# Kernel optimization log

Hardware: AMD Instinct MI355X
Metric: run time of the kernel (lower is better)

The kernel has to match this reference:

```python
import jax, jax.numpy as jnp
import numpy as np

H = 1024
NUM_HEADS = 16
HEAD_DIM = H // NUM_HEADS
EPS = 1e-6
GEN_E, GEN_IE = 8, 4096 // 8     # general experts, per-expert intermediate
MOD_E, MOD_IE = 4, 4096 // 4     # per-modality experts, per-expert intermediate


def layernorm(x, g, b):
    m = jnp.mean(x, axis=-1, keepdims=True)
    v = jnp.mean((x - m) ** 2, axis=-1, keepdims=True)
    return (x - m) * jax.lax.rsqrt(v + EPS) * g + b


def attention(x, qkv_w, qkv_b, proj_w, proj_b):
    B, N, _ = x.shape
    qkv = (x @ qkv_w + qkv_b).reshape(B, N, 3, NUM_HEADS, HEAD_DIM)
    qkv = jnp.transpose(qkv, (2, 0, 3, 1, 4))  # [3,B,h,N,d]
    q, k, v = qkv[0], qkv[1], qkv[2]
    scale = HEAD_DIM ** -0.5
    attn = jax.nn.softmax(jnp.einsum('bhnd,bhmd->bhnm', q, k) * scale, axis=-1)
    out = jnp.einsum('bhnm,bhmd->bhnd', attn, v)
    out = jnp.transpose(out, (0, 2, 1, 3)).reshape(B, N, H)
    return out @ proj_w + proj_b


def routed_mlp(x, position_ids, gate_up, down, ie):
    # expert_id = position % num_experts; compute all experts then select per token
    # (avoids materializing per-token [T,H,2I] gathered weights).
    E = gate_up.shape[0]
    eids = position_ids % E  # [B,N]
    gu = jnp.einsum('bnh,ehi->bnei', x, gate_up)              # [B,N,E,2*ie]
    gu = jnp.take_along_axis(gu, eids[..., None, None], axis=2)[:, :, 0]
    gate, up = gu[..., :ie], gu[..., ie:]
    inter = jax.nn.silu(gate) * up                             # [B,N,ie]
    dn = jnp.einsum('bni,eih->bneh', inter, down)              # [B,N,E,H]
    return jnp.take_along_axis(dn, eids[..., None, None], axis=2)[:, :, 0]


def setup_inputs() -> dict:
    key = jax.random.key(0)
    ks = jax.random.split(key, 16)
    B, N = 2, 2048
    inp = {
        'x': jax.random.normal(ks[0], (B, N, H), jnp.float32),
        'qkv_w': jax.random.normal(ks[1], (H, 3 * H), jnp.float32) * 0.02,
        'qkv_b': jnp.zeros((3 * H,), jnp.float32),
        'proj_w': jax.random.normal(ks[2], (H, H), jnp.float32) * 0.02,
        'proj_b': jnp.zeros((H,), jnp.float32),
        'ln1_g': jnp.ones((H,), jnp.float32), 'ln1_b': jnp.zeros((H,), jnp.float32),
        'ln2_g': jnp.ones((H,), jnp.float32), 'ln2_b': jnp.zeros((H,), jnp.float32),
        'ln3_g': jnp.ones((H,), jnp.float32), 'ln3_b': jnp.zeros((H,), jnp.float32),
        'gen_gu': jax.random.normal(ks[3], (GEN_E, H, 2 * GEN_IE), jnp.float32) * 0.02,
        'gen_dn': jax.random.normal(ks[4], (GEN_E, GEN_IE, H), jnp.float32) * 0.02,
        'text_gu': jax.random.normal(ks[5], (MOD_E, H, 2 * MOD_IE), jnp.float32) * 0.02,
        'text_dn': jax.random.normal(ks[6], (MOD_E, MOD_IE, H), jnp.float32) * 0.02,
        'img_gu': jax.random.normal(ks[7], (MOD_E, H, 2 * MOD_IE), jnp.float32) * 0.02,
        'img_dn': jax.random.normal(ks[8], (MOD_E, MOD_IE, H), jnp.float32) * 0.02,
        'aud_gu': jax.random.normal(ks[9], (MOD_E, H, 2 * MOD_IE), jnp.float32) * 0.02,
        'aud_dn': jax.random.normal(ks[10], (MOD_E, MOD_IE, H), jnp.float32) * 0.02,
        'vid_gu': jax.random.normal(ks[11], (MOD_E, H, 2 * MOD_IE), jnp.float32) * 0.02,
        'vid_dn': jax.random.normal(ks[12], (MOD_E, MOD_IE, H), jnp.float32) * 0.02,
        'modality_ids': jax.random.randint(ks[13], (B, N), 0, 4, jnp.int32),
        'position_ids': jnp.arange(B * N, dtype=jnp.int32).reshape(B, N),
    }
    return inp


def reference(x, qkv_w, qkv_b, proj_w, proj_b,
              ln1_g, ln1_b, ln2_g, ln2_b, ln3_g, ln3_b,
              gen_gu, gen_dn, text_gu, text_dn, img_gu, img_dn,
              aud_gu, aud_dn, vid_gu, vid_dn,
              modality_ids, position_ids):
    x = x + attention(layernorm(x, ln1_g, ln1_b), qkv_w, qkv_b, proj_w, proj_b)
    x = x + routed_mlp(layernorm(x, ln2_g, ln2_b), position_ids, gen_gu, gen_dn, GEN_IE)
    normed = layernorm(x, ln3_g, ln3_b)
    tm = (modality_ids == 0)[..., None].astype(x.dtype)
    im = (modality_ids == 1)[..., None].astype(x.dtype)
    am = (modality_ids == 2)[..., None].astype(x.dtype)
    vm = (modality_ids == 3)[..., None].astype(x.dtype)
    x = x + (routed_mlp(normed, position_ids, text_gu, text_dn, MOD_IE) * tm
             + routed_mlp(normed, position_ids, img_gu, img_dn, MOD_IE) * im
             + routed_mlp(normed, position_ids, aud_gu, aud_dn, MOD_IE) * am
             + routed_mlp(normed, position_ids, vid_gu, vid_dn, MOD_IE) * vm)
    return x
```

## Files before the change

### kernel.cpp

```cpp
#include <hip/hip_runtime.h>

#define T_TOKENS 4096
#define HDIM 1024

typedef __attribute__((ext_vector_type(8))) short bf16x8;
typedef __attribute__((ext_vector_type(4))) float f32x4;

#define EXP2F(x) __builtin_amdgcn_exp2f(x)

static __device__ inline unsigned short f2bf(float f) {
  unsigned u = __float_as_uint(f);
  unsigned r = (u + 0x7FFFu + ((u >> 16) & 1u)) >> 16;
  return (unsigned short)r;
}
static __device__ __forceinline__ unsigned cvtpk(float lo, float hi) {
  unsigned r;
  asm("v_cvt_pk_bf16_f32 %0, %1, %2" : "=v"(r) : "v"(lo), "v"(hi));
  return r;
}
static __device__ __forceinline__ void gl16(const void* g, void* l) {
  __builtin_amdgcn_global_load_lds((const __attribute__((address_space(1))) void*)g,
                                   (__attribute__((address_space(3))) void*)l, 16, 0, 0);
}

__launch_bounds__(256)
__global__ void ln_kernel(const float* __restrict__ in, const float* __restrict__ g,
                          const float* __restrict__ b, unsigned short* __restrict__ out) {
  const int row = blockIdx.x;
  const int tid = threadIdx.x;
  const long base = (long)row * HDIM;
  float4 v = *(const float4*)(in + base + tid * 4);
  __shared__ float red[256];
  red[tid] = v.x + v.y + v.z + v.w;
  __syncthreads();
  for (int st = 128; st > 0; st >>= 1) {
    if (tid < st) red[tid] += red[tid + st];
    __syncthreads();
  }
  const float mean = red[0] * (1.f / HDIM);
  __syncthreads();
  const float dx = v.x - mean, dy = v.y - mean, dz = v.z - mean, dw = v.w - mean;
  red[tid] = dx * dx + dy * dy + dz * dz + dw * dw;
  __syncthreads();
  for (int st = 128; st > 0; st >>= 1) {
    if (tid < st) red[tid] += red[tid + st];
    __syncthreads();
  }
  const float rstd = rsqrtf(red[0] * (1.f / HDIM) + 1e-6f);
  const int c = tid * 4;
  const float4 g4 = *(const float4*)(g + c);
  const float4 b4 = *(const float4*)(b + c);
  uint2 o;
  o.x = cvtpk(dx * rstd * g4.x + b4.x, dy * rstd * g4.y + b4.y);
  o.y = cvtpk(dz * rstd * g4.z + b4.z, dw * rstd * g4.w + b4.w);
  *(uint2*)(out + base + c) = o;
}

__launch_bounds__(256)
__global__ void build_groups(const int* __restrict__ pids, const int* __restrict__ mids,
                             int* __restrict__ gen_cnt, int* __restrict__ gen_list,
                             int* __restrict__ mod_cnt, int* __restrict__ mod_list) {
  const int t = blockIdx.x * 256 + threadIdx.x;
  if (t >= T_TOKENS) return;
  const int p = pids[t];
  const int ge = p & 7;
  int s = atomicAdd(&gen_cnt[ge], 1);
  if (s < 512) gen_list[ge * 512 + s] = t;
  const int g = mids[t] * 4 + (p & 3);
  s = atomicAdd(&mod_cnt[g], 1);
  if (s < 1024) mod_list[g * 1024 + s] = t;
}

__launch_bounds__(256)
__global__ void convert_w(const float* __restrict__ W, unsigned short* __restrict__ Wt,
                          int K, int N) {
  const long zo = (long)blockIdx.z * K * N;
  const float* Wp = W + zo;
  unsigned short* Wo = Wt + zo;
  const int n0 = blockIdx.x * 64, k0 = blockIdx.y * 64;
  __shared__ float T[64][65];
  const int tid = threadIdx.x;
#pragma unroll
  for (int i = 0; i < 4; ++i) {
    const int item = tid + i * 256;
    const int kk = item >> 4, c4 = (item & 15) * 4;
    const float4 v = *(const float4*)(Wp + (long)(k0 + kk) * N + n0 + c4);
    T[c4 + 0][kk] = v.x; T[c4 + 1][kk] = v.y; T[c4 + 2][kk] = v.z; T[c4 + 3][kk] = v.w;
  }
  __syncthreads();
#pragma unroll
  for (int i = 0; i < 4; ++i) {
    const int item = tid + i * 256;
    const int nn = item >> 4, k4 = (item & 15) * 4;
    uint2 p;
    p.x = cvtpk(T[nn][k4 + 0], T[nn][k4 + 1]);
    p.y = cvtpk(T[nn][k4 + 2], T[nn][k4 + 3]);
    *(uint2*)(Wo + (long)(n0 + nn) * K + k0 + k4) = p;
  }
}

enum { MODE_DENSE = 0, MODE_GEN = 1, MODE_MOD = 2 };
enum { OM_F32R = 0, OM_BF16 = 1, OM_QKV = 2 };

template <int MODE, int OMODE, bool WBF16, bool BIAS>
__launch_bounds__(256)
__global__ void mgemm(const unsigned short* __restrict__ A,
                      const void* __restrict__ w0, const float* __restrict__ w1,
                      const float* __restrict__ w2, const float* __restrict__ w3,
                      long wstep, const float* __restrict__ bias,
                      const float* __restrict__ resid, void* __restrict__ Cout,
                      unsigned short* __restrict__ qb, unsigned short* __restrict__ kb,
                      unsigned short* __restrict__ vtb,
                      int K, int N,
                      const int* __restrict__ cnts, const int* __restrict__ rowlist,
                      int cap) {
  const int z = blockIdx.z;
  const int n0 = blockIdx.x * 128;
  const int m0 = blockIdx.y * 128;

  int Meff = 1 << 30;
  const int* list = nullptr;
  if constexpr (MODE != MODE_DENSE) {
    Meff = cnts[z];
    if (m0 >= Meff) return;
    list = rowlist + z * cap;
  }

  __shared__ char As[128 * 64 * 2];
  __shared__ char Bs[128 * 64 * 2];

  const int tid = threadIdx.x;
  const int w = tid >> 6;
  const int lane = tid & 63;
  const int wm = w >> 1, wn = w & 1;
  const int srow = lane >> 3, sc = lane & 7;

  const unsigned short* asrc[4];
  char* aldsb = As + w * 4096;
#pragma unroll
  for (int i = 0; i < 4; ++i) {
    const int r = w * 32 + i * 8 + srow;
    long tok;
    if constexpr (MODE == MODE_DENSE) {
      tok = m0 + r;
    } else {
      int gm = m0 + r;
      if (gm >= Meff) gm = Meff - 1;
      tok = (long)list[gm];
    }
    asrc[i] = A + tok * (long)K + (sc ^ (r & 7)) * 8;
  }

  const unsigned short* bsrc[4];
  char* bldsb = Bs + w * 4096;
  const float* bptr[4];
  int boff[4];
  if constexpr (WBF16) {
    const unsigned short* W = (const unsigned short*)w0;
    if constexpr (MODE != MODE_DENSE) W += (long)z * wstep;
#pragma unroll
    for (int i = 0; i < 4; ++i) {
      const int r = w * 32 + i * 8 + srow;
      bsrc[i] = W + (long)(n0 + r) * K + (sc ^ (r & 7)) * 8;
    }
  } else {
    const float* W;
    if constexpr (MODE == MODE_MOD) {
      const int mm = z >> 2;
      const float* basep = (mm == 0) ? (const float*)w0 : (mm == 1) ? w1 : (mm == 2) ? w2 : w3;
      W = basep + (long)(z & 3) * wstep;
    } else {
      W = (const float*)w0 + (MODE != MODE_DENSE ? (long)z * wstep : 0);
    }
#pragma unroll
    for (int j = 0; j < 4; ++j) {
      const int item = tid + j * 256;
      const int kc = item >> 7;
      const int nl = item & 127;
      bptr[j] = W + (long)(kc * 8) * N + n0 + nl;
      boff[j] = (nl * 128 + kc * 16) ^ ((nl & 7) << 4);
    }
  }

  f32x4 acc[4][4] = {};

  for (int kt = 0; kt < K; kt += 64) {
    __syncthreads();
#pragma unroll
    for (int i = 0; i < 4; ++i) gl16(asrc[i] + kt, aldsb + i * 1024);
    if constexpr (WBF16) {
#pragma unroll
      for (int i = 0; i < 4; ++i) gl16(bsrc[i] + kt, bldsb + i * 1024);
    } else {
#pragma unroll
      for (int j = 0; j < 4; ++j) {
        const float* bp = bptr[j] + (long)kt * N;
        float kv[8];
#pragma unroll
        for (int u = 0; u < 8; ++u) kv[u] = bp[(long)u * N];
        uint4 p;
        p.x = cvtpk(kv[0], kv[1]);
        p.y = cvtpk(kv[2], kv[3]);
        p.z = cvtpk(kv[4], kv[5]);
        p.w = cvtpk(kv[6], kv[7]);
        *(uint4*)(Bs + boff[j]) = p;
      }
    }
    __syncthreads();

#pragma unroll
    for (int kk = 0; kk < 2; ++kk) {
      const int kb2 = kk * 64 + (lane >> 4) * 16;
      bf16x8 af[4], bfr[4];
#pragma unroll
      for (int f = 0; f < 4; ++f) {
        const int ar = wm * 64 + f * 16 + (lane & 15);
        af[f] = *(bf16x8*)(As + ((ar * 128 + kb2) ^ ((ar & 7) << 4)));
        const int br = wn * 64 + f * 16 + (lane & 15);
        bfr[f] = *(bf16x8*)(Bs + ((br * 128 + kb2) ^ ((br & 7) << 4)));
      }
#pragma unroll
      for (int mf = 0; mf < 4; ++mf)
#pragma unroll
        for (int nf = 0; nf < 4; ++nf)
          acc[mf][nf] =
              __builtin_amdgcn_mfma_f32_16x16x32_bf16(af[mf], bfr[nf], acc[mf][nf], 0, 0, 0);
    }
  }

  const int lr4 = (lane >> 4) * 4;
  const int lc = lane & 15;
#pragma unroll
  for (int mf = 0; mf < 4; ++mf) {
#pragma unroll
    for (int r = 0; r < 4; ++r) {
      const int gm = m0 + wm * 64 + mf * 16 + lr4 + r;
      long orow;
      if constexpr (MODE == MODE_DENSE) {
        orow = gm;
      } else {
        if (gm >= Meff) continue;
        orow = (long)list[gm];
      }
#pragma unroll
      for (int nf = 0; nf < 4; ++nf) {
        const int gc = n0 + wn * 64 + nf * 16 + lc;
        float val = acc[mf][nf][r];
        if constexpr (BIAS) val += bias[gc];
        if constexpr (OMODE == OM_F32R) {
          val += resid[orow * (long)N + gc];
          ((float*)Cout)[orow * (long)N + gc] = val;
        } else if constexpr (OMODE == OM_BF16) {
          ((unsigned short*)Cout)[orow * (long)N + gc] = f2bf(val);
        } else {
          const int bb = (int)(orow >> 11), tl = (int)orow & 2047;
          const int seg = gc >> 10, hc = gc & 1023, h = hc >> 6, d = hc & 63;
          if (seg == 0)
            qb[(((long)(bb * 16 + h) * 2048) + tl) * 64 + d] = f2bf(val * 0.18033688011112042f);
          else if (seg == 1)
            kb[(((long)(bb * 16 + h) * 2048) + tl) * 64 + d] = f2bf(val);
          else
            vtb[((long)(bb * 16 + h) * 64 + d) * 2048 + tl] = f2bf(val);
        }
      }
    }
  }
}

__launch_bounds__(256)
__global__ void attn_kernel(const unsigned short* __restrict__ Qb,
                            const unsigned short* __restrict__ Kb,
                            const unsigned short* __restrict__ Vtb,
                            unsigned short* __restrict__ out) {
  const int qt = blockIdx.x;
  const int bh = blockIdx.y;
  const int b = bh >> 4, h = bh & 15;
  const int tid = threadIdx.x;
  const int w = tid >> 6;
  const int lane = tid & 63;
  const int g = lane >> 4;
  const int q = lane & 15;

  __shared__ char Ksb[128 * 128];
  __shared__ char Vsb[64 * 256];
  __shared__ char Psb[4 * 16 * 256];
  char* Pwb = Psb + w * 4096;

  const unsigned short* Qh = Qb + ((long)(b * 16 + h) * 2048 + qt * 64) * 64;
  const unsigned short* Kh = Kb + (long)(b * 16 + h) * 2048 * 64;
  const unsigned short* Vh = Vtb + (long)(b * 16 + h) * 64 * 2048;

  bf16x8 qf[2];
#pragma unroll
  for (int kst = 0; kst < 2; ++kst)
    qf[kst] = *(const bf16x8*)(Qh + (w * 16 + q) * 64 + kst * 32 + g * 8);

  const unsigned short* ksrc[4];
  const unsigned short* vsrc[4];
  char* kld = Ksb + w * 4096;
  char* vld = Vsb + w * 4096;
#pragma unroll
  for (int i = 0; i < 4; ++i) {
    const int r = w * 32 + i * 8 + (lane >> 3);
    ksrc[i] = Kh + (long)r * 64 + ((lane & 7) ^ (r & 7)) * 8;
    const int d = w * 16 + i * 4 + (lane >> 4);
    vsrc[i] = Vh + (long)d * 2048 + ((lane & 15) ^ (d & 7)) * 8;
  }

  float m_run = -1e30f, l_run = 0.f;
  f32x4 acc[4] = {};
  const int qsw = (q & 7) << 4;

  for (int kt = 0; kt < 16; ++kt) {
    __syncthreads();
#pragma unroll
    for (int i = 0; i < 4; ++i) gl16(ksrc[i] + (long)kt * 128 * 64, kld + i * 1024);
#pragma unroll
    for (int i = 0; i < 4; ++i) gl16(vsrc[i] + kt * 128, vld + i * 1024);
    __syncthreads();

    f32x4 sf[8];
#pragma unroll
    for (int f = 0; f < 8; ++f) {
      const int krow = f * 16 + q;
      const int sw = (krow & 7) << 4;
      const bf16x8 k0 = *(bf16x8*)(Ksb + krow * 128 + ((g * 16) ^ sw));
      const bf16x8 k1 = *(bf16x8*)(Ksb + krow * 128 + ((64 + g * 16) ^ sw));
      f32x4 t = {};
      t = __builtin_amdgcn_mfma_f32_16x16x32_bf16(k0, qf[0], t, 0, 0, 0);
      sf[f] = __builtin_amdgcn_mfma_f32_16x16x32_bf16(k1, qf[1], t, 0, 0, 0);
    }

    float mx = sf[0][0];
#pragma unroll
    for (int f = 0; f < 8; ++f) {
      mx = fmaxf(mx, fmaxf(fmaxf(sf[f][0], sf[f][1]), fmaxf(sf[f][2], sf[f][3])));
    }
    mx = fmaxf(mx, __shfl_xor(mx, 16));
    mx = fmaxf(mx, __shfl_xor(mx, 32));
    const float mn = fmaxf(m_run, mx);
    const float alpha = EXP2F(m_run - mn);
    m_run = mn;

    float ls = 0.f;
#pragma unroll
    for (int f = 0; f < 8; ++f) {
#pragma unroll
      for (int r = 0; r < 4; ++r) {
        sf[f][r] = EXP2F(sf[f][r] - mn);
      }
      ls += (sf[f][0] + sf[f][1]) + (sf[f][2] + sf[f][3]);
    }
    ls += __shfl_xor(ls, 16);
    ls += __shfl_xor(ls, 32);
    l_run = l_run * alpha + ls;

#pragma unroll
    for (int f = 0; f < 8; ++f) {
      const unsigned p0 = cvtpk(sf[f][0], sf[f][1]);
      const unsigned p1 = cvtpk(sf[f][2], sf[f][3]);
      const int base = f * 32 + g * 8;
      *(unsigned*)(Pwb + q * 256 + ((base) ^ qsw)) = p0;
      *(unsigned*)(Pwb + q * 256 + ((base + 4) ^ qsw)) = p1;
    }

#pragma unroll
    for (int r = 0; r < 4; ++r) {
      const float aO = __shfl(alpha, g * 4 + r, 64);
      acc[0][r] *= aO; acc[1][r] *= aO; acc[2][r] *= aO; acc[3][r] *= aO;
    }

#pragma unroll
    for (int kst = 0; kst < 4; ++kst) {
      const bf16x8 pa = *(bf16x8*)(Pwb + q * 256 + ((kst * 64 + g * 16) ^ qsw));
#pragma unroll
      for (int df = 0; df < 4; ++df) {
        const int vrow = df * 16 + q;
        const int vsw = (vrow & 7) << 4;
        const bf16x8 vf = *(bf16x8*)(Vsb + vrow * 256 + ((kst * 64 + g * 16) ^ vsw));
        acc[df] = __builtin_amdgcn_mfma_f32_16x16x32_bf16(pa, vf, acc[df], 0, 0, 0);
      }
    }
  }

  float linv[4];
#pragma unroll
  for (int r = 0; r < 4; ++r) linv[r] = 1.f / __shfl(l_run, g * 4 + r, 64);
  unsigned short* op = out + (long)(b * 2048 + qt * 64 + w * 16) * 1024 + h * 64;
#pragma unroll
  for (int df = 0; df < 4; ++df)
#pragma unroll
    for (int r = 0; r < 4; ++r) {
      const int row = g * 4 + r;
      op[(long)row * 1024 + df * 16 + q] = f2bf(acc[df][r] * linv[r]);
    }
}

__launch_bounds__(256)
__global__ void silu_bf(const unsigned short* __restrict__ gu, unsigned short* __restrict__ inter,
                        int IE2, int IE, int shift) {
  const int total = T_TOKENS << shift;
  for (int idx = blockIdx.x * 256 + threadIdx.x; idx < total; idx += gridDim.x * 256) {
    const int t = idx >> shift;
    const int r8 = (idx & ((1 << shift) - 1)) * 8;
    const unsigned short* gp = gu + (long)t * IE2 + r8;
    const uint4 gg = *(const uint4*)gp;
    const uint4 uu = *(const uint4*)(gp + IE);
    const unsigned gw[4] = {gg.x, gg.y, gg.z, gg.w};
    const unsigned uw[4] = {uu.x, uu.y, uu.z, uu.w};
    uint4 o;
    unsigned ow[4];
#pragma unroll
    for (int qq = 0; qq < 4; ++qq) {
      const float g0 = __uint_as_float(gw[qq] << 16);
      const float g1 = __uint_as_float(gw[qq] & 0xffff0000u);
      const float u0 = __uint_as_float(uw[qq] << 16);
      const float u1 = __uint_as_float(uw[qq] & 0xffff0000u);
      const float r0 = g0 / (1.f + __expf(-g0)) * u0;
      const float r1 = g1 / (1.f + __expf(-g1)) * u1;
      ow[qq] = cvtpk(r0, r1);
    }
    o.x = ow[0]; o.y = ow[1]; o.z = ow[2]; o.w = ow[3];
    *(uint4*)(inter + (long)t * IE + r8) = o;
  }
}

extern "C" void kernel_launch(void* const* d_in, const int* in_sizes, int n_in,
                              void* d_out, int out_size, void* d_ws, size_t ws_size,
                              hipStream_t stream) {
  const float* x       = (const float*)d_in[0];
  const float* qkv_w   = (const float*)d_in[1];
  const float* qkv_b   = (const float*)d_in[2];
  const float* proj_w  = (const float*)d_in[3];
  const float* proj_b  = (const float*)d_in[4];
  const float* ln1_g   = (const float*)d_in[5];
  const float* ln1_b   = (const float*)d_in[6];
  const float* ln2_g   = (const float*)d_in[7];
  const float* ln2_b   = (const float*)d_in[8];
  const float* ln3_g   = (const float*)d_in[9];
  const float* ln3_b   = (const float*)d_in[10];
  const float* gen_gu  = (const float*)d_in[11];
  const float* gen_dn  = (const float*)d_in[12];
  const float* text_gu = (const float*)d_in[13];
  const float* text_dn = (const float*)d_in[14];
  const float* img_gu  = (const float*)d_in[15];
  const float* img_dn  = (const float*)d_in[16];
  const float* aud_gu  = (const float*)d_in[17];
  const float* aud_dn  = (const float*)d_in[18];
  const float* vid_gu  = (const float*)d_in[19];
  const float* vid_dn  = (const float*)d_in[20];
  const int* mids      = (const int*)d_in[21];
  const int* pids      = (const int*)d_in[22];
  float* out = (float*)d_out;
  char* ws = (char*)d_ws;

  const unsigned long MB = 1ul << 20;
  unsigned short* lnb   = (unsigned short*)(ws);
  unsigned short* Qb    = (unsigned short*)(ws + 8 * MB);
  unsigned short* Kb    = (unsigned short*)(ws + 16 * MB);
  unsigned short* Vtb   = (unsigned short*)(ws + 24 * MB);
  unsigned short* attno = (unsigned short*)(ws + 32 * MB);
  unsigned short* wqkv  = (unsigned short*)(ws + 40 * MB);
  unsigned short* wproj = (unsigned short*)(ws + 46 * MB);
  unsigned short* wggu  = (unsigned short*)(ws + 48 * MB);
  unsigned short* wgdn  = (unsigned short*)(ws + 64 * MB);
  int* gen_cnt  = (int*)(ws + 72 * MB);
  int* mod_cnt  = gen_cnt + 8;
  int* gen_list = gen_cnt + 32;
  int* mod_list = gen_list + 8 * 512;
  unsigned short* guo    = Qb;
  unsigned short* intero = Vtb;

  (void)hipMemsetAsync(gen_cnt, 0, (8 + 16) * sizeof(int), stream);
  build_groups<<<16, 256, 0, stream>>>(pids, mids, gen_cnt, gen_list, mod_cnt, mod_list);

  convert_w<<<dim3(48, 16, 1), 256, 0, stream>>>(qkv_w, wqkv, 1024, 3072);
  convert_w<<<dim3(16, 16, 1), 256, 0, stream>>>(proj_w, wproj, 1024, 1024);
  convert_w<<<dim3(16, 16, 8), 256, 0, stream>>>(gen_gu, wggu, 1024, 1024);
  convert_w<<<dim3(16, 8, 8), 256, 0, stream>>>(gen_dn, wgdn, 512, 1024);

  ln_kernel<<<4096, 256, 0, stream>>>(x, ln1_g, ln1_b, lnb);
  mgemm<MODE_DENSE, OM_QKV, true, true><<<dim3(24, 32, 1), 256, 0, stream>>>(
      lnb, wqkv, nullptr, nullptr, nullptr, 0L, qkv_b, nullptr, nullptr,
      Qb, Kb, Vtb, 1024, 3072, nullptr, nullptr, 0);
  attn_kernel<<<dim3(32, 32, 1), 256, 0, stream>>>(Qb, Kb, Vtb, attno);
  mgemm<MODE_DENSE, OM_F32R, true, true><<<dim3(8, 32, 1), 256, 0, stream>>>(
      attno, wproj, nullptr, nullptr, nullptr, 0L, proj_b, x, out,
      nullptr, nullptr, nullptr, 1024, 1024, nullptr, nullptr, 0);

  ln_kernel<<<4096, 256, 0, stream>>>(out, ln2_g, ln2_b, lnb);
  mgemm<MODE_GEN, OM_BF16, true, false><<<dim3(8, 4, 8), 256, 0, stream>>>(
      lnb, wggu, nullptr, nullptr, nullptr, (long)1024 * 1024, nullptr, nullptr, guo,
      nullptr, nullptr, nullptr, 1024, 1024, gen_cnt, gen_list, 512);
  silu_bf<<<1024, 256, 0, stream>>>(guo, intero, 1024, 512, 6);
  mgemm<MODE_GEN, OM_F32R, true, false><<<dim3(8, 4, 8), 256, 0, stream>>>(
      intero, wgdn, nullptr, nullptr, nullptr, (long)1024 * 512, nullptr, out, out,
      nullptr, nullptr, nullptr, 512, 1024, gen_cnt, gen_list, 512);

  ln_kernel<<<4096, 256, 0, stream>>>(out, ln3_g, ln3_b, lnb);
  mgemm<MODE_MOD, OM_BF16, false, false><<<dim3(16, 8, 16), 256, 0, stream>>>(
      lnb, text_gu, img_gu, aud_gu, vid_gu, (long)1024 * 2048, nullptr, nullptr, guo,
      nullptr, nullptr, nullptr, 1024, 2048, mod_cnt, mod_list, 1024);
  silu_bf<<<2048, 256, 0, stream>>>(guo, intero, 2048, 1024, 7);
  mgemm<MODE_MOD, OM_F32R, false, false><<<dim3(8, 8, 16), 256, 0, stream>>>(
      intero, text_dn, img_dn, aud_dn, vid_dn, (long)1024 * 1024, nullptr, out, out,
      nullptr, nullptr, nullptr, 1024, 1024, mod_cnt, mod_list, 1024);
}
```

Before: 417.3 us.

## Double-buffer GEMM LDS tiles to overlap global loads with MFMA compute

```diff
diff --git a/kernel.cpp b/kernel.cpp
--- a/kernel.cpp
+++ b/kernel.cpp
@@ -126,8 +126,9 @@
     list = rowlist + z * cap;
   }
 
-  __shared__ char As[128 * 64 * 2];
-  __shared__ char Bs[128 * 64 * 2];
+  constexpr int BUFSZ = 128 * 64 * 2;
+  __shared__ char As[2 * BUFSZ];
+  __shared__ char Bs[2 * BUFSZ];
 
   const int tid = threadIdx.x;
   const int w = tid >> 6;
@@ -136,7 +137,6 @@
   const int srow = lane >> 3, sc = lane & 7;
 
   const unsigned short* asrc[4];
-  char* aldsb = As + w * 4096;
 #pragma unroll
   for (int i = 0; i < 4; ++i) {
     const int r = w * 32 + i * 8 + srow;
@@ -152,7 +152,6 @@
   }
 
   const unsigned short* bsrc[4];
-  char* bldsb = Bs + w * 4096;
   const float* bptr[4];
   int boff[4];
   if constexpr (WBF16) {
@@ -183,31 +182,36 @@
   }
 
   f32x4 acc[4][4] = {};
-
-  for (int kt = 0; kt < K; kt += 64) {
-    __syncthreads();
-#pragma unroll
-    for (int i = 0; i < 4; ++i) gl16(asrc[i] + kt, aldsb + i * 1024);
-    if constexpr (WBF16) {
-#pragma unroll
-      for (int i = 0; i < 4; ++i) gl16(bsrc[i] + kt, bldsb + i * 1024);
-    } else {
-#pragma unroll
-      for (int j = 0; j < 4; ++j) {
-        const float* bp = bptr[j] + (long)kt * N;
-        float kv[8];
-#pragma unroll
-        for (int u = 0; u < 8; ++u) kv[u] = bp[(long)u * N];
-        uint4 p;
-        p.x = cvtpk(kv[0], kv[1]);
-        p.y = cvtpk(kv[2], kv[3]);
-        p.z = cvtpk(kv[4], kv[5]);
-        p.w = cvtpk(kv[6], kv[7]);
-        *(uint4*)(Bs + boff[j]) = p;
-      }
-    }
-    __syncthreads();
-
+  float kv[4][8];
+
+  auto stageA = [&](int s, int kt) {
+#pragma unroll
+    for (int i = 0; i < 4; ++i) gl16(asrc[i] + kt, As + s * BUFSZ + w * 4096 + i * 1024);
+  };
+  auto stageB16 = [&](int s, int kt) {
+#pragma unroll
+    for (int i = 0; i < 4; ++i) gl16(bsrc[i] + kt, Bs + s * BUFSZ + w * 4096 + i * 1024);
+  };
+  auto loadB = [&](int kt) {
+#pragma unroll
+    for (int j = 0; j < 4; ++j) {
+      const float* bp = bptr[j] + (long)kt * N;
+#pragma unroll
+      for (int u = 0; u < 8; ++u) kv[j][u] = bp[(long)u * N];
+    }
+  };
+  auto writeB = [&](int s) {
+#pragma unroll
+    for (int j = 0; j < 4; ++j) {
+      uint4 p;
+      p.x = cvtpk(kv[j][0], kv[j][1]);
+      p.y = cvtpk(kv[j][2], kv[j][3]);
+      p.z = cvtpk(kv[j][4], kv[j][5]);
+      p.w = cvtpk(kv[j][6], kv[j][7]);
+      *(uint4*)(Bs + s * BUFSZ + boff[j]) = p;
+    }
+  };
+  auto compute = [&](int s) {
 #pragma unroll
     for (int kk = 0; kk < 2; ++kk) {
       const int kb2 = kk * 64 + (lane >> 4) * 16;
@@ -215,9 +219,9 @@
 #pragma unroll
       for (int f = 0; f < 4; ++f) {
         const int ar = wm * 64 + f * 16 + (lane & 15);
-        af[f] = *(bf16x8*)(As + ((ar * 128 + kb2) ^ ((ar & 7) << 4)));
+        af[f] = *(bf16x8*)(As + s * BUFSZ + ((ar * 128 + kb2) ^ ((ar & 7) << 4)));
         const int br = wn * 64 + f * 16 + (lane & 15);
-        bfr[f] = *(bf16x8*)(Bs + ((br * 128 + kb2) ^ ((br & 7) << 4)));
+        bfr[f] = *(bf16x8*)(Bs + s * BUFSZ + ((br * 128 + kb2) ^ ((br & 7) << 4)));
       }
 #pragma unroll
       for (int mf = 0; mf < 4; ++mf)
@@ -226,6 +230,33 @@
           acc[mf][nf] =
               __builtin_amdgcn_mfma_f32_16x16x32_bf16(af[mf], bfr[nf], acc[mf][nf], 0, 0, 0);
     }
+  };
+
+  const int nk = K >> 6;
+  stageA(0, 0);
+  if constexpr (WBF16) {
+    stageB16(0, 0);
+  } else {
+    loadB(0);
+    writeB(0);
+  }
+  __syncthreads();
+
+  int sel = 0;
+  for (int t = 0; t < nk; ++t) {
+    const bool more = (t + 1) < nk;
+    const int ktn = (t + 1) * 64;
+    if (more) {
+      stageA(sel ^ 1, ktn);
+      if constexpr (WBF16) stageB16(sel ^ 1, ktn);
+      else loadB(ktn);
+    }
+    compute(sel);
+    if constexpr (!WBF16) {
+      if (more) writeB(sel ^ 1);
+    }
+    __syncthreads();
+    sel ^= 1;
   }
 
   const int lr4 = (lane >> 4) * 4;
```

Result: faster. 385.0 us (-7.7%).
